# Performance work log

Measured on AMD Instinct MI355X. Metric: run time of the kernel, lower is better.

## Reference

```python
import jax, jax.numpy as jnp
import numpy as np

NB_IN, NB_REC, NB_OUT = 256, 1024, 64
B, NB_STEPS = 128, 300
NOISE_SCALE = 0.05
TIME_STEP, TAU_MEM, TAU_SYN = 0.001, 0.01, 0.005
ALPHA = float(np.exp(-TIME_STEP / TAU_SYN))
BETA = float(np.exp(-TIME_STEP / TAU_MEM))
WEIGHT_SCALE = 7.0 * (1.0 - BETA)


def setup_inputs() -> dict:
    key = jax.random.key(0)
    k0, k1, k2, k3, k4, k5 = jax.random.split(key, 6)
    inputs = jax.random.normal(k0, (B, NB_STEPS, NB_IN), jnp.float32)
    noise = NOISE_SCALE * jax.random.normal(k1, (B, NB_STEPS, NB_REC), jnp.float32)
    w_ff = (WEIGHT_SCALE / np.sqrt(NB_IN)) * jax.random.normal(k2, (NB_IN, NB_REC), jnp.float32)
    w_rec = (WEIGHT_SCALE / np.sqrt(NB_REC)) * jax.random.normal(k3, (NB_REC, NB_REC), jnp.float32)
    w_out = (WEIGHT_SCALE / np.sqrt(NB_REC)) * jax.random.normal(k4, (NB_REC, NB_OUT), jnp.float32)
    # Dale sign vector: +/-1 per recurrent neuron (diag of D_sign), p=0.5 each
    d_sign = jnp.where(jax.random.bernoulli(k5, 0.5, (NB_REC,)), 1.0, -1.0).astype(jnp.float32)
    return {"inputs": inputs, "noise": noise, "w_ff": w_ff, "w_rec": w_rec,
            "w_out": w_out, "d_sign": d_sign}


def reference(inputs, noise, w_ff, w_rec, w_out, d_sign):
    # Dale's law: rectify weights, then sign rows by D_sign (torch.mm(D_sign, W))
    w_rec_d = d_sign[:, None] * jnp.abs(w_rec)   # [R, R]
    w_out_d = d_sign[:, None] * jnp.abs(w_out)   # [R, O]

    in_ff = jnp.einsum('btc,cd->btd', inputs, w_ff)  # [B, T, R]
    T = NB_STEPS - 1  # loop iterations in the original

    # time-major sequences for scan
    in_seq = jnp.swapaxes(in_ff[:, :T, :], 0, 1)     # [T, B, R]
    nz_seq = jnp.swapaxes(noise[:, :T, :], 0, 1)     # [T, B, R]

    zeros_br = jnp.zeros((B, NB_REC), jnp.float32)

    def step(carry, xs):
        syn, mem, rst1, rst2 = carry  # rst1 = reset from t-1, rst2 = from t-2
        in_t, nz_t = xs
        # hard reset for neurons that spiked in either of the two previous steps
        mem = jnp.where((rst1 > 0) | (rst2 > 0), 0.0, mem)
        mthr = mem - 1.0
        out = (mthr > 0).astype(mem.dtype)           # spike (SuperSpike fwd = heaviside)
        rst = out                                    # rst[c]=1 where mthr>0
        rec = out @ w_rec_d                          # [B, R]
        new_syn = ALPHA * syn + rec + in_t + nz_t
        new_mem = BETA * mem + syn - rst             # uses OLD syn, as in original
        h2 = out @ w_out_d                           # [B, O]
        return (new_syn, new_mem, rst, rst1), (new_mem, out, h2)

    carry0 = (zeros_br, zeros_br, zeros_br, zeros_br)
    _, (mem_seq, spk_seq, h2_seq) = jax.lax.scan(step, carry0, (in_seq, nz_seq))

    # prepend the t=0 records (mem=0 for spk_rec, h2=0 for out_rec), batch-major
    spk_rec = jnp.concatenate([zeros_br[None], spk_seq], axis=0).swapaxes(0, 1)  # [B, T+1, R]
    out0 = jnp.zeros((1, B, NB_OUT), jnp.float32)
    out_rec = jnp.concatenate([out0, h2_seq], axis=0).swapaxes(0, 1)             # [B, T+1, O]

    return out_rec, spk_rec, w_rec_d, w_out_d, w_ff
```

## Files before the change

kernel.cpp:

```cpp
#include <hip/hip_runtime.h>


constexpr int NB_IN  = 256;
constexpr int NB_REC = 1024;
constexpr int NB_OUT = 64;
constexpr int BATCH  = 128;
constexpr int NB_STEPS = 300;
constexpr int TSTEPS = NB_STEPS - 1;

constexpr float ALPHA_F = (float)0.8187307530779818;
constexpr float BETA_F  = (float)0.9048374180359595;

constexpr size_t OUT_REC_OFF = 0;
constexpr size_t SPK_REC_OFF = (size_t)BATCH * NB_STEPS * NB_OUT;
constexpr size_t WRECD_OFF   = SPK_REC_OFF + (size_t)BATCH * NB_STEPS * NB_REC;
constexpr size_t WOUTD_OFF   = WRECD_OFF + (size_t)NB_REC * NB_REC;
constexpr size_t WFF_OFF     = WOUTD_OFF + (size_t)NB_REC * NB_OUT;
constexpr int    OUT_TOTAL   = 43155456;

constexpr int SZ_INPUTS = BATCH * NB_STEPS * NB_IN;
constexpr int SZ_NOISE  = BATCH * NB_STEPS * NB_REC;
constexpr int SZ_WFF    = NB_IN * NB_REC;
constexpr int SZ_WREC   = NB_REC * NB_REC;
constexpr int SZ_WOUT   = NB_REC * NB_OUT;
constexpr int SZ_DSIGN  = NB_REC;

constexpr int WREC_ROWS = NB_REC + 1;

__global__ void sentinel_kernel(float* out, float v) { out[0] = v; }

__global__ void weights_kernel(const float* __restrict__ w_rec,
                               const float* __restrict__ w_out,
                               const float* __restrict__ w_ff,
                               const float* __restrict__ d_sign,
                               float* __restrict__ f_wrecd,
                               float* __restrict__ f_woutd,
                               float* __restrict__ o_wrecd,
                               float* __restrict__ o_woutd,
                               float* __restrict__ o_wff) {
  int idx = blockIdx.x * blockDim.x + threadIdx.x;
  if (idx < NB_REC * NB_REC) {
    int i = idx >> 10;
    float v = d_sign[i] * fabsf(w_rec[idx]);
    f_wrecd[idx] = v;
    o_wrecd[idx] = v;
    return;
  }
  int idx2 = idx - NB_REC * NB_REC;
  if (idx2 < NB_REC * NB_OUT) {
    int i = idx2 >> 6;
    float v = d_sign[i] * fabsf(w_out[idx2]);
    f_woutd[idx2] = v;
    o_woutd[idx2] = v;
    return;
  }
  int idx3 = idx2 - NB_REC * NB_OUT;
  if (idx3 < NB_IN * NB_REC) {
    o_wff[idx3] = w_ff[idx3];
    return;
  }
  int idx4 = idx3 - NB_IN * NB_REC;
  if (idx4 < NB_REC) {
    f_wrecd[(size_t)NB_REC * NB_REC + idx4] = 0.0f;
  }
}

__global__ __launch_bounds__(256)
void inff_einsum(const float* __restrict__ A,
                 const float* __restrict__ Bw,
                 float* __restrict__ C,
                 int rows) {
  const int r0 = blockIdx.x * 8;
  const int d  = blockIdx.y * 256 + threadIdx.x;

  __shared__ float a_s[8][NB_IN];
  for (int e = threadIdx.x; e < 8 * NB_IN; e += 256) {
    int rr = e >> 8, cc = e & 255;
    a_s[rr][cc] = (r0 + rr < rows) ? A[(size_t)(r0 + rr) * NB_IN + cc] : 0.0f;
  }
  __syncthreads();

  float acc[8] = {0.f, 0.f, 0.f, 0.f, 0.f, 0.f, 0.f, 0.f};
  for (int c = 0; c < NB_IN; ++c) {
    const float w = Bw[(size_t)c * NB_REC + d];
#pragma unroll
    for (int rr = 0; rr < 8; ++rr)
      acc[rr] = __fadd_rn(acc[rr], __fmul_rn(a_s[rr][c], w));
  }
#pragma unroll
  for (int rr = 0; rr < 8; ++rr)
    if (r0 + rr < rows) C[(size_t)(r0 + rr) * NB_REC + d] = acc[rr];
}

__global__ __launch_bounds__(1024, 1)
void rnn_kernel(const float* __restrict__ inff,
                const float* __restrict__ noise,
                const float* __restrict__ w_rec_d,
                float* __restrict__ spk_rec) {
  const int b = blockIdx.x;
  const int j = threadIdx.x;
  const int lane = j & 63;
  const int wv = j >> 6;

  __shared__ unsigned s_mask[2][32];
  __shared__ uint4 sidx4_s[16][136];

  unsigned short* sidxw = (unsigned short*)sidx4_s[wv];
  const uint4* sidx4w = (const uint4*)sidx4_s[wv];

  float syn = 0.0f, mem = 0.0f;
  int rst1 = 0, rst2 = 0;

  spk_rec[((size_t)b * NB_STEPS) * NB_REC + j] = 0.0f;

  const float* wc = w_rec_d + j;

  float inf = inff[((size_t)b * NB_STEPS) * NB_REC + j];
  float nz  = noise[((size_t)b * NB_STEPS) * NB_REC + j];

  for (int t = 0; t < TSTEPS; ++t) {
    const int p = t & 1;
    const size_t row = (size_t)b * NB_STEPS + t;

    const float mem_eff = (rst1 | rst2) ? 0.0f : mem;
    const int spike = (__fsub_rn(mem_eff, 1.0f) > 0.0f) ? 1 : 0;

    const unsigned long long msk = __ballot(spike);
    if (lane == 0) {
      s_mask[p][2 * wv]     = (unsigned)msk;
      s_mask[p][2 * wv + 1] = (unsigned)(msk >> 32);
    }

    const float infn = inff[(row + 1) * NB_REC + j];
    const float nzn  = noise[(row + 1) * NB_REC + j];

    __syncthreads();

    const unsigned m0 = (lane < 32) ? s_mask[p][lane] : 0u;
    const int pc = __popc(m0);
    int x = pc;
#pragma unroll
    for (int d = 1; d < 64; d <<= 1) {
      int y = __shfl_up(x, (unsigned)d, 64);
      if (lane >= d) x += y;
    }
    int base = x - pc;
    unsigned m = m0;
    while (m) {
      const int bit = __builtin_ctz(m);
      m &= m - 1;
      sidxw[base++] = (unsigned short)((lane << 5) + bit);
    }
    const int S = __shfl(x, 63);
    if (lane < 48) sidxw[S + lane] = (unsigned short)NB_REC;

    auto load16 = [&](int k, float* buf) {
      const uint4 p0 = sidx4w[(k >> 3) + 0];
      const uint4 p1 = sidx4w[(k >> 3) + 1];
      const unsigned e[16] = {
          p0.x & 0xffffu, p0.x >> 16, p0.y & 0xffffu, p0.y >> 16,
          p0.z & 0xffffu, p0.z >> 16, p0.w & 0xffffu, p0.w >> 16,
          p1.x & 0xffffu, p1.x >> 16, p1.y & 0xffffu, p1.y >> 16,
          p1.z & 0xffffu, p1.z >> 16, p1.w & 0xffffu, p1.w >> 16};
#pragma unroll
      for (int q = 0; q < 16; ++q)
        buf[q] = wc[(size_t)e[q] << 10];
    };

    float acc = 0.0f;
    float bufA[16], bufB[16];
    load16(0, bufA);
    for (int k0 = 0; k0 < S; k0 += 32) {
      load16(k0 + 16, bufB);
#pragma unroll
      for (int q = 0; q < 16; ++q) acc = __fadd_rn(acc, bufA[q]);
      load16(k0 + 32, bufA);
#pragma unroll
      for (int q = 0; q < 16; ++q) acc = __fadd_rn(acc, bufB[q]);
    }

    const float new_syn =
        __fadd_rn(__fadd_rn(__fadd_rn(__fmul_rn(ALPHA_F, syn), acc), inf), nz);
    const float new_mem =
        __fsub_rn(__fadd_rn(__fmul_rn(BETA_F, mem_eff), syn), (float)spike);

    spk_rec[(row + 1) * NB_REC + j] = (float)spike;

    syn = new_syn;
    mem = new_mem;
    rst2 = rst1;
    rst1 = spike;
    inf = infn;
    nz = nzn;
  }
}

__global__ __launch_bounds__(256)
void h2_kernel(const float* __restrict__ spk_rec,
               const float* __restrict__ w_out_d,
               float* __restrict__ out_rec,
               int nrows) {
  const int r = blockIdx.x * 4 + (threadIdx.x >> 6);
  const int lane = threadIdx.x & 63;
  if (r >= nrows) return;

  const float* spk = spk_rec + (size_t)r * NB_REC;
  const float* wo  = w_out_d + lane;

  unsigned long long mw[16];
#pragma unroll
  for (int c = 0; c < 16; ++c)
    mw[c] = __ballot(spk[c * 64 + lane] != 0.0f);

  float acc = 0.0f;
#pragma unroll
  for (int c = 0; c < 16; ++c) {
    unsigned long long m = mw[c];
    while (m) {
      float w[8];
#pragma unroll
      for (int q = 0; q < 8; ++q) {
        const bool v = (m != 0ull);
        const int idx = v ? __builtin_ctzll(m) : 0;
        m &= m - 1ull;
        const float ld = wo[(size_t)(v ? (c * 64 + idx) : 0) << 6];
        w[q] = v ? ld : 0.0f;
      }
#pragma unroll
      for (int q = 0; q < 8; ++q) acc = __fadd_rn(acc, w[q]);
    }
  }
  out_rec[(size_t)r * NB_OUT + lane] = acc;
}

extern "C" void kernel_launch(void* const* d_in, const int* in_sizes, int n_in,
                              void* d_out, int out_size, void* d_ws, size_t ws_size,
                              hipStream_t stream) {
  const float *inputs = nullptr, *noise = nullptr, *w_ff = nullptr,
              *w_rec = nullptr, *w_out = nullptr, *d_sign = nullptr;
  for (int i = 0; i < n_in; ++i) {
    switch (in_sizes[i]) {
      case SZ_INPUTS: inputs = (const float*)d_in[i]; break;
      case SZ_NOISE:  noise  = (const float*)d_in[i]; break;
      case SZ_WFF:    w_ff   = (const float*)d_in[i]; break;
      case SZ_WREC:   w_rec  = (const float*)d_in[i]; break;
      case SZ_WOUT:   w_out  = (const float*)d_in[i]; break;
      case SZ_DSIGN:  d_sign = (const float*)d_in[i]; break;
      default: break;
    }
  }

  float* out = (float*)d_out;
  const size_t W_ELEMS = (size_t)WREC_ROWS * NB_REC + SZ_WOUT;
  const size_t W_BYTES = W_ELEMS * sizeof(float);

  float sentinel = 0.0f;
  if (!inputs || !noise || !w_ff || !w_rec || !w_out || !d_sign) {
    sentinel = 300.0f;
  } else if (out_size != OUT_TOTAL) {
    sentinel = 700.0f;
  }

  int CB = 0;
  if (sentinel == 0.0f) {
    const int cands[4] = {128, 64, 32, 16};
    for (int i = 0; i < 4; ++i) {
      size_t need = W_BYTES + (size_t)cands[i] * NB_STEPS * NB_REC * sizeof(float);
      if (need <= ws_size) { CB = cands[i]; break; }
    }
    if (CB == 0) sentinel = 500.0f + (float)(ws_size >> 20);
  }

  if (sentinel != 0.0f) {
    sentinel_kernel<<<1, 1, 0, stream>>>(out, sentinel);
    return;
  }

  float* out_rec = out + OUT_REC_OFF;
  float* spk_rec = out + SPK_REC_OFF;
  float* o_wrecd = out + WRECD_OFF;
  float* o_woutd = out + WOUTD_OFF;
  float* o_wff   = out + WFF_OFF;

  float* f_wrecd = (float*)d_ws;
  float* f_woutd = f_wrecd + (size_t)WREC_ROWS * NB_REC;
  float* inff    = f_woutd + SZ_WOUT;

  {
    int total = NB_REC * NB_REC + NB_REC * NB_OUT + NB_IN * NB_REC + NB_REC;
    int blocks = (total + 255) / 256;
    weights_kernel<<<blocks, 256, 0, stream>>>(w_rec, w_out, w_ff, d_sign,
                                               f_wrecd, f_woutd,
                                               o_wrecd, o_woutd, o_wff);
  }

  for (int b0 = 0; b0 < BATCH; b0 += CB) {
    const int cb = (BATCH - b0 < CB) ? (BATCH - b0) : CB;
    const int rows = cb * NB_STEPS;
    const float* Aptr = inputs + (size_t)b0 * NB_STEPS * NB_IN;
    const float* Nptr = noise + (size_t)b0 * NB_STEPS * NB_REC;
    float* srec = spk_rec + (size_t)b0 * NB_STEPS * NB_REC;

    dim3 ggrid((rows + 7) / 8, NB_REC / 256);
    inff_einsum<<<ggrid, 256, 0, stream>>>(Aptr, w_ff, inff, rows);
    rnn_kernel<<<cb, 1024, 0, stream>>>(inff, Nptr, f_wrecd, srec);
  }

  {
    const int nrows = BATCH * NB_STEPS;
    h2_kernel<<<(nrows + 3) / 4, 256, 0, stream>>>(spk_rec, f_woutd,
                                                   out_rec, nrows);
  }
}
```

Baseline: 2.218 ms.

## Store spike masks in workspace for h2, use byte offsets in recurrent gather

```diff
diff --git a/kernel.cpp b/kernel.cpp
--- a/kernel.cpp
+++ b/kernel.cpp
@@ -26,6 +26,7 @@
 constexpr int SZ_DSIGN  = NB_REC;
 
 constexpr int WREC_ROWS = NB_REC + 1;
+constexpr int NROWS     = BATCH * NB_STEPS;
 
 __global__ void sentinel_kernel(float* out, float v) { out[0] = v; }
 
@@ -34,7 +35,6 @@
                                const float* __restrict__ w_ff,
                                const float* __restrict__ d_sign,
                                float* __restrict__ f_wrecd,
-                               float* __restrict__ f_woutd,
                                float* __restrict__ o_wrecd,
                                float* __restrict__ o_woutd,
                                float* __restrict__ o_wff) {
@@ -49,9 +49,7 @@
   int idx2 = idx - NB_REC * NB_REC;
   if (idx2 < NB_REC * NB_OUT) {
     int i = idx2 >> 6;
-    float v = d_sign[i] * fabsf(w_out[idx2]);
-    f_woutd[idx2] = v;
-    o_woutd[idx2] = v;
+    o_woutd[idx2] = d_sign[i] * fabsf(w_out[idx2]);
     return;
   }
   int idx3 = idx2 - NB_REC * NB_OUT;
@@ -96,24 +94,26 @@
 void rnn_kernel(const float* __restrict__ inff,
                 const float* __restrict__ noise,
                 const float* __restrict__ w_rec_d,
-                float* __restrict__ spk_rec) {
+                float* __restrict__ spk_rec,
+                unsigned long long* __restrict__ gws) {
   const int b = blockIdx.x;
   const int j = threadIdx.x;
   const int lane = j & 63;
   const int wv = j >> 6;
 
   __shared__ unsigned s_mask[2][32];
-  __shared__ uint4 sidx4_s[16][136];
-
-  unsigned short* sidxw = (unsigned short*)sidx4_s[wv];
-  const uint4* sidx4w = (const uint4*)sidx4_s[wv];
+  __shared__ uint4 soff4[16][272];
+
+  unsigned* soffw = (unsigned*)soff4[wv];
+  const uint4* soff4w = soff4[wv];
 
   float syn = 0.0f, mem = 0.0f;
   int rst1 = 0, rst2 = 0;
 
   spk_rec[((size_t)b * NB_STEPS) * NB_REC + j] = 0.0f;
 
-  const float* wc = w_rec_d + j;
+  const char* wbase = (const char*)w_rec_d;
+  const unsigned jb = (unsigned)(j << 2);
 
   float inf = inff[((size_t)b * NB_STEPS) * NB_REC + j];
   float nz  = noise[((size_t)b * NB_STEPS) * NB_REC + j];
@@ -129,8 +129,10 @@
     if (lane == 0) {
       s_mask[p][2 * wv]     = (unsigned)msk;
       s_mask[p][2 * wv + 1] = (unsigned)(msk >> 32);
-    }
-
+      if (gws) gws[(row + 1) * 16 + wv] = msk;
+    }
+
+    spk_rec[(row + 1) * NB_REC + j] = (float)spike;
     const float infn = inff[(row + 1) * NB_REC + j];
     const float nzn  = noise[(row + 1) * NB_REC + j];
 
@@ -149,22 +151,21 @@
     while (m) {
       const int bit = __builtin_ctz(m);
       m &= m - 1;
-      sidxw[base++] = (unsigned short)((lane << 5) + bit);
+      soffw[base++] = (unsigned)(((lane << 5) + bit) << 12);
     }
     const int S = __shfl(x, 63);
-    if (lane < 48) sidxw[S + lane] = (unsigned short)NB_REC;
+    if (lane < 48) soffw[S + lane] = (unsigned)(NB_REC << 12);
 
     auto load16 = [&](int k, float* buf) {
-      const uint4 p0 = sidx4w[(k >> 3) + 0];
-      const uint4 p1 = sidx4w[(k >> 3) + 1];
-      const unsigned e[16] = {
-          p0.x & 0xffffu, p0.x >> 16, p0.y & 0xffffu, p0.y >> 16,
-          p0.z & 0xffffu, p0.z >> 16, p0.w & 0xffffu, p0.w >> 16,
-          p1.x & 0xffffu, p1.x >> 16, p1.y & 0xffffu, p1.y >> 16,
-          p1.z & 0xffffu, p1.z >> 16, p1.w & 0xffffu, p1.w >> 16};
+      const uint4 o0 = soff4w[(k >> 2) + 0];
+      const uint4 o1 = soff4w[(k >> 2) + 1];
+      const uint4 o2 = soff4w[(k >> 2) + 2];
+      const uint4 o3 = soff4w[(k >> 2) + 3];
+      const unsigned e[16] = {o0.x, o0.y, o0.z, o0.w, o1.x, o1.y, o1.z, o1.w,
+                              o2.x, o2.y, o2.z, o2.w, o3.x, o3.y, o3.z, o3.w};
 #pragma unroll
       for (int q = 0; q < 16; ++q)
-        buf[q] = wc[(size_t)e[q] << 10];
+        buf[q] = *reinterpret_cast<const float*>(wbase + (size_t)(e[q] + jb));
     };
 
     float acc = 0.0f;
@@ -183,8 +184,6 @@
         __fadd_rn(__fadd_rn(__fadd_rn(__fmul_rn(ALPHA_F, syn), acc), inf), nz);
     const float new_mem =
         __fsub_rn(__fadd_rn(__fmul_rn(BETA_F, mem_eff), syn), (float)spike);
-
-    spk_rec[(row + 1) * NB_REC + j] = (float)spike;
 
     syn = new_syn;
     mem = new_mem;
@@ -196,10 +195,51 @@
 }
 
 __global__ __launch_bounds__(256)
-void h2_kernel(const float* __restrict__ spk_rec,
-               const float* __restrict__ w_out_d,
-               float* __restrict__ out_rec,
-               int nrows) {
+void h2_fast(const unsigned long long* __restrict__ gws,
+             const float* __restrict__ w_out_d,
+             float* __restrict__ out_rec,
+             int nrows) {
+  const int r = blockIdx.x * 4 + (threadIdx.x >> 6);
+  const int lane = threadIdx.x & 63;
+  if (r >= nrows) return;
+  if (r % NB_STEPS == 0) {
+    out_rec[(size_t)r * NB_OUT + lane] = 0.0f;
+    return;
+  }
+
+  const unsigned long long* mrow = gws + (size_t)r * 16;
+  unsigned long long mw[16];
+#pragma unroll
+  for (int c = 0; c < 16; ++c) mw[c] = mrow[c];
+
+  const float* wo = w_out_d + lane;
+
+  float acc = 0.0f;
+#pragma unroll
+  for (int c = 0; c < 16; ++c) {
+    unsigned long long m = mw[c];
+    while (m) {
+      float w[8];
+#pragma unroll
+      for (int q = 0; q < 8; ++q) {
+        const bool v = (m != 0ull);
+        const int idx = v ? __builtin_ctzll(m) : 0;
+        m &= m - 1ull;
+        const float ld = wo[(size_t)(v ? (c * 64 + idx) : 0) << 6];
+        w[q] = v ? ld : 0.0f;
+      }
+#pragma unroll
+      for (int q = 0; q < 8; ++q) acc = __fadd_rn(acc, w[q]);
+    }
+  }
+  out_rec[(size_t)r * NB_OUT + lane] = acc;
+}
+
+__global__ __launch_bounds__(256)
+void h2_slow(const float* __restrict__ spk_rec,
+             const float* __restrict__ w_out_d,
+             float* __restrict__ out_rec,
+             int nrows) {
   const int r = blockIdx.x * 4 + (threadIdx.x >> 6);
   const int lane = threadIdx.x & 63;
   if (r >= nrows) return;
@@ -251,30 +291,30 @@
   }
 
   float* out = (float*)d_out;
-  const size_t W_ELEMS = (size_t)WREC_ROWS * NB_REC + SZ_WOUT;
-  const size_t W_BYTES = W_ELEMS * sizeof(float);
+
+  const size_t WREC_ELEMS = (size_t)WREC_ROWS * NB_REC;
+  const size_t WREC_BYTES = WREC_ELEMS * sizeof(float);
+  const size_t GWS_BYTES  = (size_t)NROWS * 16 * 8;
+  const size_t INFF_BYTES = (size_t)NROWS * NB_REC * sizeof(float);
+
+  const size_t need_fast = WREC_BYTES + GWS_BYTES + INFF_BYTES;
+  const size_t need_slow = WREC_BYTES + INFF_BYTES;
 
   float sentinel = 0.0f;
   if (!inputs || !noise || !w_ff || !w_rec || !w_out || !d_sign) {
     sentinel = 300.0f;
   } else if (out_size != OUT_TOTAL) {
     sentinel = 700.0f;
-  }
-
-  int CB = 0;
-  if (sentinel == 0.0f) {
-    const int cands[4] = {128, 64, 32, 16};
-    for (int i = 0; i < 4; ++i) {
-      size_t need = W_BYTES + (size_t)cands[i] * NB_STEPS * NB_REC * sizeof(float);
-      if (need <= ws_size) { CB = cands[i]; break; }
-    }
-    if (CB == 0) sentinel = 500.0f + (float)(ws_size >> 20);
+  } else if (need_slow > ws_size) {
+    sentinel = 500.0f + (float)(ws_size >> 20);
   }
 
   if (sentinel != 0.0f) {
     sentinel_kernel<<<1, 1, 0, stream>>>(out, sentinel);
     return;
   }
+
+  const bool fast = (need_fast <= ws_size);
 
   float* out_rec = out + OUT_REC_OFF;
   float* spk_rec = out + SPK_REC_OFF;
@@ -283,32 +323,30 @@
   float* o_wff   = out + WFF_OFF;
 
   float* f_wrecd = (float*)d_ws;
-  float* f_woutd = f_wrecd + (size_t)WREC_ROWS * NB_REC;
-  float* inff    = f_woutd + SZ_WOUT;
+  unsigned long long* gws =
+      fast ? (unsigned long long*)(f_wrecd + WREC_ELEMS) : nullptr;
+  float* inff = fast ? (float*)(gws + (size_t)NROWS * 16)
+                     : (f_wrecd + WREC_ELEMS);
 
   {
     int total = NB_REC * NB_REC + NB_REC * NB_OUT + NB_IN * NB_REC + NB_REC;
     int blocks = (total + 255) / 256;
     weights_kernel<<<blocks, 256, 0, stream>>>(w_rec, w_out, w_ff, d_sign,
-                                               f_wrecd, f_woutd,
+                                               f_wrecd,
                                                o_wrecd, o_woutd, o_wff);
   }
 
-  for (int b0 = 0; b0 < BATCH; b0 += CB) {
-    const int cb = (BATCH - b0 < CB) ? (BATCH - b0) : CB;
-    const int rows = cb * NB_STEPS;
-    const float* Aptr = inputs + (size_t)b0 * NB_STEPS * NB_IN;
-    const float* Nptr = noise + (size_t)b0 * NB_STEPS * NB_REC;
-    float* srec = spk_rec + (size_t)b0 * NB_STEPS * NB_REC;
-
-    dim3 ggrid((rows + 7) / 8, NB_REC / 256);
-    inff_einsum<<<ggrid, 256, 0, stream>>>(Aptr, w_ff, inff, rows);
-    rnn_kernel<<<cb, 1024, 0, stream>>>(inff, Nptr, f_wrecd, srec);
-  }
-
   {
-    const int nrows = BATCH * NB_STEPS;
-    h2_kernel<<<(nrows + 3) / 4, 256, 0, stream>>>(spk_rec, f_woutd,
-                                                   out_rec, nrows);
-  }
-}
+    dim3 ggrid((NROWS + 7) / 8, NB_REC / 256);
+    inff_einsum<<<ggrid, 256, 0, stream>>>(inputs, w_ff, inff, NROWS);
+  }
+
+  rnn_kernel<<<BATCH, 1024, 0, stream>>>(inff, noise, f_wrecd, spk_rec, gws);
+
+  if (fast) {
+    h2_fast<<<(NROWS + 3) / 4, 256, 0, stream>>>(gws, o_woutd, out_rec, NROWS);
+  } else {
+    h2_slow<<<(NROWS + 3) / 4, 256, 0, stream>>>(spk_rec, o_woutd,
+                                                 out_rec, NROWS);
+  }
+}
```

Result: no change. 2.214 ms (-0.2%).
